# Kernel optimization log

Measured on AMD Instinct MI355X. Metric: run time of the kernel, lower is better.

## Reference

```python
import jax, jax.numpy as jnp
import numpy as np
import math

FACTOR = 100.0
WN_THRESH = 0.99

# extra MANO palm-closing faces from the original module
FACES_NEW = np.array([[92, 38, 234], [234, 38, 239], [38, 122, 239], [239, 122, 279],
                      [122, 118, 279], [279, 118, 215], [118, 117, 215], [215, 117, 214],
                      [117, 119, 214], [214, 119, 121], [119, 120, 121], [121, 120, 78],
                      [120, 108, 78], [78, 108, 79]], dtype=np.int64)


def solid_angles(points, triangles):
    # points: (B,Q,3); triangles: (B,F,3,3) -> (B,Q,F)
    ct = triangles[:, None] - points[:, :, None, None]        # (B,Q,F,3,3)
    norms = jnp.linalg.norm(ct, axis=-1)                      # (B,Q,F,3)
    cross = jnp.cross(ct[..., 1, :], ct[..., 2, :])           # (B,Q,F,3)
    numerator = jnp.sum(ct[..., 0, :] * cross, axis=-1)       # (B,Q,F)
    dot01 = jnp.sum(ct[..., 0, :] * ct[..., 1, :], axis=-1)
    dot12 = jnp.sum(ct[..., 1, :] * ct[..., 2, :], axis=-1)
    dot02 = jnp.sum(ct[..., 0, :] * ct[..., 2, :], axis=-1)
    denominator = (norms.prod(axis=-1) + dot01 * norms[..., 2]
                   + dot02 * norms[..., 1] + dot12 * norms[..., 0])
    return 2.0 * jnp.arctan2(numerator, denominator)


def winding_numbers(points, triangles):
    return solid_angles(points, triangles).sum(axis=-1) / (4.0 * math.pi)


def pairwise_dist(x, y, squared=False):
    # x: (B,N,3), y: (B,M,3) -> (B,N,M)
    xx = jnp.sum(x * x, axis=-1)
    yy = jnp.sum(y * y, axis=-1)
    zz = jnp.einsum('bnd,bmd->bnm', x, y)
    P = xx[:, :, None] + yy[:, None, :] - 2.0 * zz
    if not squared:
        P = jnp.sqrt(jnp.clip(P, 0.0))
    return P


def setup_inputs() -> dict:
    key = jax.random.key(0)
    k1, k2, k3 = jax.random.split(key, 3)
    B, Q, NF = 8, 778, 1538
    v1 = jax.random.normal(k1, (B, Q, 3), dtype=jnp.float32)
    v2 = jax.random.normal(k2, (B, Q, 3), dtype=jnp.float32)
    faces = jax.random.randint(k3, (NF, 3), 0, Q, dtype=jnp.int64)
    return {"v1": v1, "v2": v2, "faces": faces}


def reference(v1, v2, faces):
    r_faces = jnp.concatenate([faces, jnp.asarray(FACES_NEW)], axis=0)   # (F,3)
    l_faces = r_faces[:, jnp.array([0, 2, 1])]
    t1l = v1[:, l_faces, :]   # (B,F,3,3)
    t2l = v2[:, r_faces, :]
    interior_v1 = winding_numbers(v1, t2l) >= WN_THRESH   # (B,Q) bool
    interior_v2 = winding_numbers(v2, t1l) >= WN_THRESH

    d12 = pairwise_dist(v1, v2)       # (B,Q,Q)
    d21 = pairwise_dist(v2, v1)
    min12 = jnp.min(d12, axis=-1)     # (B,Q): dist from each v1 point to v2
    min21 = jnp.min(d21, axis=-1)

    pt1 = ((min12 * FACTOR) ** 2) * interior_v1.astype(v1.dtype)
    pt2 = ((min21 * FACTOR) ** 2) * interior_v2.astype(v2.dtype)
    bloss = pt1.sum(axis=-1) + pt2.sum(axis=-1)   # (B,)
    gate = jnp.any(interior_v1, axis=-1) & jnp.any(interior_v2, axis=-1)
    bloss = jnp.where(gate, bloss, 0.0)
    return bloss.mean()
```

## Files before the change

kernel.cpp:

```cpp
#include <hip/hip_runtime.h>
#include <math.h>

#define BQ 778
#define NF_IN 1538
#define NF_NEW 14
#define NT 1552
#define NB 8
#define BLOCK 512
#define PTS_PER_BLOCK 8

__constant__ int FACES_NEW_D[NF_NEW * 3] = {
    92, 38, 234, 234, 38, 239, 38, 122, 239, 239, 122, 279,
    122, 118, 279, 279, 118, 215, 118, 117, 215, 215, 117, 214,
    117, 119, 214, 214, 119, 121, 119, 120, 121, 121, 120, 78,
    120, 108, 78, 78, 108, 79};

__device__ __forceinline__ float fast_atan2f(float y, float x) {
  float ax = __builtin_fabsf(x), ay = __builtin_fabsf(y);
  float mx = fmaxf(ax, ay), mn = fminf(ax, ay);
  float r  = __builtin_amdgcn_rcpf(mx);
  float t  = mn * r;
  float e  = __builtin_fmaf(-t, mx, mn);
  t = __builtin_fmaf(e, r, t);
  float s = t * t;
  float u =                  0.00282363896258175373077393f;
  u = __builtin_fmaf(u, s, -0.0159569028764963150024414f);
  u = __builtin_fmaf(u, s,  0.0425049886107444763183594f);
  u = __builtin_fmaf(u, s, -0.0748900920152664184570312f);
  u = __builtin_fmaf(u, s,  0.106347933411598205566406f);
  u = __builtin_fmaf(u, s, -0.142027363181114196777344f);
  u = __builtin_fmaf(u, s,  0.199926957488059997558594f);
  u = __builtin_fmaf(u, s, -0.333331018686294555664062f);
  float a = __builtin_fmaf(u * s, t, t);
  a = (ay > ax) ? (1.57079632679489662f - a) : a;
  a = (x < 0.0f) ? (3.14159265358979323f - a) : a;
  return __builtin_copysignf(a, y);
}

__global__ __launch_bounds__(BLOCK) void wn_dist_kernel(
    const float* __restrict__ v1, const float* __restrict__ v2,
    const int* __restrict__ faces, float* __restrict__ sums,
    unsigned int* __restrict__ flags) {
  __shared__ float4 sv[BQ];
  __shared__ ushort4 sf4[NT];

  const int BPC = (BQ + PTS_PER_BLOCK - 1) / PTS_PER_BLOCK;
  int bid = blockIdx.x;
  int cloud = bid / BPC;
  int qbase = (bid % BPC) * PTS_PER_BLOCK;
  int side = cloud >> 3;
  int b = cloud & 7;

  const float* pts = (side == 0) ? (v1 + b * BQ * 3) : (v2 + b * BQ * 3);
  const float* opp = (side == 0) ? (v2 + b * BQ * 3) : (v1 + b * BQ * 3);

  int tid = threadIdx.x;
  for (int i = tid; i < BQ; i += BLOCK) {
    sv[i] = make_float4(opp[i * 3 + 0], opp[i * 3 + 1], opp[i * 3 + 2], 0.0f);
  }
  for (int f = tid; f < NF_IN; f += BLOCK) {
    ushort4 u;
    u.x = (unsigned short)(faces[f * 3 + 0] << 4);
    u.y = (unsigned short)(faces[f * 3 + 1] << 4);
    u.z = (unsigned short)(faces[f * 3 + 2] << 4);
    u.w = 0;
    sf4[f] = u;
  }
  for (int f = tid; f < NF_NEW; f += BLOCK) {
    ushort4 u;
    u.x = (unsigned short)(FACES_NEW_D[f * 3 + 0] << 4);
    u.y = (unsigned short)(FACES_NEW_D[f * 3 + 1] << 4);
    u.z = (unsigned short)(FACES_NEW_D[f * 3 + 2] << 4);
    u.w = 0;
    sf4[NF_IN + f] = u;
  }
  __syncthreads();

  int wave = tid >> 6;
  int lane = tid & 63;
  int q = qbase + wave;
  if (q >= BQ) return;

  const float sgn = side ? -1.0f : 1.0f;
  float px = pts[q * 3 + 0];
  float py = pts[q * 3 + 1];
  float pz = pts[q * 3 + 2];

  const char* svb = (const char*)sv;

  float omega = 0.0f;
  for (int t = lane; t < NT; t += 64) {
    ushort4 f = sf4[t];
    float4 va = *(const float4*)(svb + f.x);
    float4 vb = *(const float4*)(svb + f.y);
    float4 vc = *(const float4*)(svb + f.z);
    float ax = va.x - px, ay = va.y - py, az = va.z - pz;
    float bx = vb.x - px, by = vb.y - py, bz = vb.z - pz;
    float cx = vc.x - px, cy = vc.y - py, cz = vc.z - pz;
    float la = sqrtf(ax * ax + ay * ay + az * az);
    float lb = sqrtf(bx * bx + by * by + bz * bz);
    float lc = sqrtf(cx * cx + cy * cy + cz * cz);
    float crx = by * cz - bz * cy;
    float cry = bz * cx - bx * cz;
    float crz = bx * cy - by * cx;
    float num = ax * crx + ay * cry + az * crz;
    float d01 = ax * bx + ay * by + az * bz;
    float d02 = ax * cx + ay * cy + az * cz;
    float d12 = bx * cx + by * cy + bz * cz;
    float den = la * lb * lc + d01 * lc + d02 * lb + d12 * la;
    omega += fast_atan2f(sgn * num, den);
  }

  float dmin = 3.402823466e38f;
  for (int j = lane; j < BQ; j += 64) {
    float4 vj = sv[j];
    float dx = vj.x - px, dy = vj.y - py, dz = vj.z - pz;
    float d2 = dx * dx + dy * dy + dz * dz;
    dmin = fminf(dmin, d2);
  }

  for (int off = 32; off; off >>= 1) {
    omega += __shfl_xor(omega, off);
    dmin = fminf(dmin, __shfl_xor(dmin, off));
  }

  if (lane == 0) {
    float wn = omega * 0.15915494309189535f;
    bool interior = (wn >= 0.99f);
    if (interior) {
      float pt = fmaxf(dmin, 0.0f) * 10000.0f;
      atomicAdd(&sums[cloud], pt);
      atomicOr(&flags[cloud], 1u);
    }
  }
}

__global__ void finalize_kernel(const float* __restrict__ sums,
                                const unsigned int* __restrict__ flags,
                                float* __restrict__ out) {
  if (threadIdx.x == 0) {
    float total = 0.0f;
    for (int b = 0; b < NB; ++b) {
      bool gate = (flags[b] != 0u) && (flags[NB + b] != 0u);
      if (gate) total += sums[b] + sums[NB + b];
    }
    out[0] = total * (1.0f / NB);
  }
}

extern "C" void kernel_launch(void* const* d_in, const int* in_sizes, int n_in,
                              void* d_out, int out_size, void* d_ws,
                              size_t ws_size, hipStream_t stream) {
  const float* v1 = (const float*)d_in[0];
  const float* v2 = (const float*)d_in[1];
  const int* faces = (const int*)d_in[2];
  float* out = (float*)d_out;

  float* sums = (float*)d_ws;
  unsigned int* flags = (unsigned int*)(sums + 16);

  hipMemsetAsync(d_ws, 0, 16 * sizeof(float) + 16 * sizeof(unsigned int),
                 stream);

  const int BPC = (BQ + PTS_PER_BLOCK - 1) / PTS_PER_BLOCK;
  int grid = 2 * NB * BPC;
  wn_dist_kernel<<<grid, BLOCK, 0, stream>>>(v1, v2, faces, sums, flags);
  finalize_kernel<<<1, 64, 0, stream>>>(sums, flags, out);
}
```

Measured before the change: 138.7 us.

## Map query points to lanes and split triangles across waves with LDS reduction

Each block now handles 64 query points, one per lane, while the 16 waves of a 1024-thread block each take a contiguous slice of 97 triangles and a strided slice of the nearest-neighbour search. Triangle and vertex reads from LDS become wave-uniform broadcasts instead of per-lane gathers. Partial winding sums and minimum distances are combined through shared memory, followed by one shuffle reduction and one atomic per block. The grid shrinks from 1552 blocks to 208, which cuts the repeated LDS setup of vertices and faces. In exchange, there are fewer blocks than CUs and a block-wide barrier is added.

```diff
diff --git a/kernel.cpp b/kernel.cpp
--- a/kernel.cpp
+++ b/kernel.cpp
@@ -6,8 +6,9 @@
 #define NF_NEW 14
 #define NT 1552
 #define NB 8
-#define BLOCK 512
-#define PTS_PER_BLOCK 8
+#define BLOCK 1024
+#define NWAVE 16
+#define TRI_PER_WAVE 97
 
 __constant__ int FACES_NEW_D[NF_NEW * 3] = {
     92, 38, 234, 234, 38, 239, 38, 122, 239, 239, 122, 279,
@@ -43,11 +44,13 @@
     unsigned int* __restrict__ flags) {
   __shared__ float4 sv[BQ];
   __shared__ ushort4 sf4[NT];
+  __shared__ float romega[NWAVE][64];
+  __shared__ float rdmin[NWAVE][64];
 
-  const int BPC = (BQ + PTS_PER_BLOCK - 1) / PTS_PER_BLOCK;
+  const int PG = 13;
   int bid = blockIdx.x;
-  int cloud = bid / BPC;
-  int qbase = (bid % BPC) * PTS_PER_BLOCK;
+  int cloud = bid / PG;
+  int pg = bid % PG;
   int side = cloud >> 3;
   int b = cloud & 7;
 
@@ -78,19 +81,21 @@
 
   int wave = tid >> 6;
   int lane = tid & 63;
-  int q = qbase + wave;
-  if (q >= BQ) return;
+  int q = pg * 64 + lane;
+  bool valid = (q < BQ);
+  int qc = valid ? q : (BQ - 1);
 
   const float sgn = side ? -1.0f : 1.0f;
-  float px = pts[q * 3 + 0];
-  float py = pts[q * 3 + 1];
-  float pz = pts[q * 3 + 2];
+  float px = pts[qc * 3 + 0];
+  float py = pts[qc * 3 + 1];
+  float pz = pts[qc * 3 + 2];
 
   const char* svb = (const char*)sv;
 
   float omega = 0.0f;
-  for (int t = lane; t < NT; t += 64) {
-    ushort4 f = sf4[t];
+  int tbase = wave * TRI_PER_WAVE;
+  for (int k = 0; k < TRI_PER_WAVE; ++k) {
+    ushort4 f = sf4[tbase + k];
     float4 va = *(const float4*)(svb + f.x);
     float4 vb = *(const float4*)(svb + f.y);
     float4 vc = *(const float4*)(svb + f.z);
@@ -112,25 +117,32 @@
   }
 
   float dmin = 3.402823466e38f;
-  for (int j = lane; j < BQ; j += 64) {
+  for (int j = wave; j < BQ; j += NWAVE) {
     float4 vj = sv[j];
     float dx = vj.x - px, dy = vj.y - py, dz = vj.z - pz;
-    float d2 = dx * dx + dy * dy + dz * dz;
-    dmin = fminf(dmin, d2);
+    dmin = fminf(dmin, dx * dx + dy * dy + dz * dz);
   }
 
-  for (int off = 32; off; off >>= 1) {
-    omega += __shfl_xor(omega, off);
-    dmin = fminf(dmin, __shfl_xor(dmin, off));
-  }
+  romega[wave][lane] = omega;
+  rdmin[wave][lane] = dmin;
+  __syncthreads();
 
-  if (lane == 0) {
-    float wn = omega * 0.15915494309189535f;
-    bool interior = (wn >= 0.99f);
-    if (interior) {
-      float pt = fmaxf(dmin, 0.0f) * 10000.0f;
+  if (wave == 0) {
+    float om = 0.0f;
+    float dm = 3.402823466e38f;
+#pragma unroll
+    for (int w = 0; w < NWAVE; ++w) {
+      om += romega[w][lane];
+      dm = fminf(dm, rdmin[w][lane]);
+    }
+    float wn = om * 0.15915494309189535f;
+    bool interior = valid && (wn >= 0.99f);
+    float pt = interior ? fmaxf(dm, 0.0f) * 10000.0f : 0.0f;
+    for (int off = 32; off; off >>= 1) pt += __shfl_xor(pt, off);
+    bool anyint = __any(interior);
+    if (lane == 0) {
       atomicAdd(&sums[cloud], pt);
-      atomicOr(&flags[cloud], 1u);
+      if (anyint) atomicOr(&flags[cloud], 1u);
     }
   }
 }
@@ -162,8 +174,7 @@
   hipMemsetAsync(d_ws, 0, 16 * sizeof(float) + 16 * sizeof(unsigned int),
                  stream);
 
-  const int BPC = (BQ + PTS_PER_BLOCK - 1) / PTS_PER_BLOCK;
-  int grid = 2 * NB * BPC;
+  int grid = 16 * 13;
   wn_dist_kernel<<<grid, BLOCK, 0, stream>>>(v1, v2, faces, sums, flags);
   finalize_kernel<<<1, 64, 0, stream>>>(sums, flags, out);
 }
```

Result: slower. 150.2 us (+8.3%).
